# Performance work log

Measured on AMD Instinct MI355X. Metric: run time of the kernel, lower is better.

The kernel has to match this reference:

```python
import jax, jax.numpy as jnp
import numpy as np

N, B, H, L0, L1, C = 196608, 4096, 230, 10, 53, 53


def setup_inputs() -> dict:
    key = jax.random.key(0)
    ks = jax.random.split(key, 12)
    x = jax.random.normal(ks[0], (N, H), jnp.float32)
    label_index = jax.random.randint(ks[1], (N,), 0, C, dtype=jnp.int32)
    rl0 = jax.random.randint(ks[2], (C, 1), 0, L0, dtype=jnp.int32)
    rl1 = jax.random.randint(ks[3], (C, 1), 0, L1, dtype=jnp.int32)
    relation_levels = jnp.concatenate([rl0, rl1], axis=1)  # [C, 2]
    # equal-size bags: 4096 bags of 48 sentences (ragged boundaries)
    scope = (jnp.arange(B + 1, dtype=jnp.int32) * (N // B))
    rel_emb0 = jax.random.normal(ks[4], (L0, H), jnp.float32)
    rel_emb1 = jax.random.normal(ks[5], (L1, H), jnp.float32)
    att_w0 = jax.random.normal(ks[6], (L0,), jnp.float32)
    att_w1 = jax.random.normal(ks[7], (L1,), jnp.float32)
    w_s = jax.random.normal(ks[8], (2, 3 * H), jnp.float32) * 0.05
    b_s = jax.random.normal(ks[9], (2, 1), jnp.float32) * 0.05
    disc_matrix = jax.random.normal(ks[10], (C, 2 * H), jnp.float32) * 0.05
    bias = jnp.zeros((C,), jnp.float32)
    return {"x": x, "rel_emb0": rel_emb0, "rel_emb1": rel_emb1,
            "att_w0": att_w0, "att_w1": att_w1, "w_s": w_s, "b_s": b_s,
            "disc_matrix": disc_matrix, "bias": bias,
            "label_index": label_index, "relation_levels": relation_levels,
            "scope": scope}


def _segment_softmax(logits, seg, num_seg):
    # logits: [N]; stable softmax within each bag (segment)
    m = jax.ops.segment_max(logits, seg, num_segments=num_seg)
    e = jnp.exp(logits - m[seg])
    z = jax.ops.segment_sum(e, seg, num_segments=num_seg)
    return e / z[seg]


def reference(x, rel_emb0, rel_emb1, att_w0, att_w1, w_s, b_s, disc_matrix,
              bias, label_index, relation_levels, scope):
    n, h = x.shape
    num_bags = scope.shape[0] - 1
    # bag id of each sentence from ragged boundaries
    seg = jnp.searchsorted(scope, jnp.arange(n, dtype=scope.dtype), side="right") - 1

    ll = relation_levels[label_index]                 # [N, 2]
    r0 = rel_emb0[ll[:, 0]]                           # [N, H]
    r1 = rel_emb1[ll[:, 1]]                           # [N, H]
    s = jnp.tanh(jnp.concatenate([x, r0, r1], axis=-1))  # [N, 3H]
    logits = w_s @ s.T + b_s                          # [2, N]

    # per-bag ragged softmax over sentences, per hierarchy level
    score = jax.vmap(lambda l: _segment_softmax(l, seg, num_bags))(logits)  # [2, N]

    # vertical (hierarchy) attention: softmax over hier per sentence, mean per bag
    v = jnp.stack([att_w0[ll[:, 0]], att_w1[ll[:, 1]]])  # [2, N]
    vsm = jax.nn.softmax(v, axis=0)                      # [2, N]
    counts = jax.ops.segment_sum(jnp.ones((n,), x.dtype), seg, num_segments=num_bags)
    layer_att = jax.vmap(lambda r: jax.ops.segment_sum(r, seg, num_segments=num_bags))(vsm) / counts  # [2, B]

    # attention-weighted bag representation: per bag, [2, len] @ [len, H]
    rep = jax.vmap(lambda sc: jax.ops.segment_sum(sc[:, None] * x, seg, num_segments=num_bags))(score)  # [2, B, H]
    tower = (layer_att[:, :, None] * rep).transpose(1, 0, 2).reshape(num_bags, 2 * h)  # [B, 2H]

    return tower @ disc_matrix.T + bias  # [B, C]
```

## Files before the change

### kernel.cpp

```cpp
#include <hip/hip_runtime.h>

#define NTOT 196608
#define BAGS 4096
#define H 230
#define H3 690
#define NC 53

__device__ __forceinline__ float fast_tanh(float x) {
    float e = __expf(2.f * x);
    float r = __builtin_amdgcn_rcpf(e + 1.f);
    return fmaf(-2.f, r, 1.f);
}

__global__ void class_table_kernel(const float* __restrict__ rel_emb0,
                                   const float* __restrict__ rel_emb1,
                                   const float* __restrict__ att_w0,
                                   const float* __restrict__ att_w1,
                                   const float* __restrict__ w_s,
                                   const float* __restrict__ b_s,
                                   const int* __restrict__ relation_levels,
                                   float* __restrict__ cls)
{
    int c = blockIdx.x;
    int lane = threadIdx.x;
    int l0 = relation_levels[c * 2 + 0];
    int l1 = relation_levels[c * 2 + 1];
    float a00 = 0.f, a01 = 0.f, a10 = 0.f, a11 = 0.f;
    for (int j = lane; j < H; j += 64) {
        float t0 = fast_tanh(rel_emb0[l0 * H + j]);
        float t1 = fast_tanh(rel_emb1[l1 * H + j]);
        a00 += w_s[0 * H3 + H + j] * t0;
        a01 += w_s[0 * H3 + 2 * H + j] * t1;
        a10 += w_s[1 * H3 + H + j] * t0;
        a11 += w_s[1 * H3 + 2 * H + j] * t1;
    }
    for (int m = 32; m; m >>= 1) {
        a00 += __shfl_xor(a00, m);
        a01 += __shfl_xor(a01, m);
        a10 += __shfl_xor(a10, m);
        a11 += __shfl_xor(a11, m);
    }
    if (lane == 0) {
        cls[0 * NC + c] = a00 + a01 + b_s[0];
        cls[1 * NC + c] = a10 + a11 + b_s[1];
        float v0 = att_w0[l0], v1 = att_w1[l1];
        float mx = fmaxf(v0, v1);
        float e0 = __expf(v0 - mx), e1 = __expf(v1 - mx);
        float rz = __builtin_amdgcn_rcpf(e0 + e1);
        cls[2 * NC + c] = e0 * rz;
        cls[3 * NC + c] = e1 * rz;
    }
}

__global__ __launch_bounds__(256, 8) void bag_kernel(
    const float* __restrict__ x,
    const float* __restrict__ w_s,
    const float* __restrict__ disc,
    const float* __restrict__ bias,
    const int* __restrict__ label_index,
    const int* __restrict__ scope,
    const float* __restrict__ cls,
    float* __restrict__ out)
{
    __shared__ __align__(16) float part[4][464];
    __shared__ float zs[4][4];
    __shared__ __align__(16) float t01[464];

    int b = blockIdx.x;
    int start = scope[b];
    int cnt = scope[b + 1] - start;
    int tid = threadIdx.x;
    int wave = tid >> 6;
    int lane = tid & 63;
    const float* xb = x + (long long)start * H;

    float w0r[4], w1r[4];
#pragma unroll
    for (int u = 0; u < 4; ++u) {
        int jj = lane + 64 * u;
        w0r[u] = (jj < H) ? w_s[jj] : 0.f;
        w1r[u] = (jj < H) ? w_s[H3 + jj] : 0.f;
    }

    float acc0[4] = {0.f, 0.f, 0.f, 0.f};
    float acc1[4] = {0.f, 0.f, 0.f, 0.f};
    float z0 = 0.f, z1 = 0.f, sv0 = 0.f, sv1 = 0.f;

    for (int t = 0; t < 12; ++t) {
        int i = wave + 4 * t;
        if (i >= cnt) break;
        const float* row = xb + i * H;
        float r[4];
        float d0 = 0.f, d1 = 0.f;
#pragma unroll
        for (int u = 0; u < 4; ++u) {
            int jj = lane + 64 * u;
            r[u] = (jj < H) ? row[jj] : 0.f;
        }
#pragma unroll
        for (int u = 0; u < 4; ++u) {
            float tnh = fast_tanh(r[u]);
            d0 += w0r[u] * tnh;
            d1 += w1r[u] * tnh;
        }
#pragma unroll
        for (int m = 32; m; m >>= 1) {
            d0 += __shfl_xor(d0, m);
            d1 += __shfl_xor(d1, m);
        }
        int c = label_index[start + i];
        float e0 = __expf(d0 + cls[c]);
        float e1 = __expf(d1 + cls[NC + c]);
        z0 += e0; z1 += e1;
        sv0 += cls[2 * NC + c];
        sv1 += cls[3 * NC + c];
#pragma unroll
        for (int u = 0; u < 4; ++u) {
            acc0[u] = fmaf(e0, r[u], acc0[u]);
            acc1[u] = fmaf(e1, r[u], acc1[u]);
        }
    }

#pragma unroll
    for (int u = 0; u < 4; ++u) {
        int jj = lane + 64 * u;
        if (jj < H) {
            part[wave][jj]     = acc0[u];
            part[wave][H + jj] = acc1[u];
        }
    }
    if (lane == 0) {
        zs[wave][0] = z0; zs[wave][1] = z1;
        zs[wave][2] = sv0; zs[wave][3] = sv1;
    }
    __syncthreads();

    float zt0 = zs[0][0] + zs[1][0] + zs[2][0] + zs[3][0];
    float zt1 = zs[0][1] + zs[1][1] + zs[2][1] + zs[3][1];
    float st0 = zs[0][2] + zs[1][2] + zs[2][2] + zs[3][2];
    float st1 = zs[0][3] + zs[1][3] + zs[2][3] + zs[3][3];
    float rc  = __builtin_amdgcn_rcpf((float)cnt);
    float s0  = st0 * rc * __builtin_amdgcn_rcpf(zt0);
    float s1  = st1 * rc * __builtin_amdgcn_rcpf(zt1);

    for (int t = tid; t < 2 * H; t += 256) {
        float s = part[0][t] + part[1][t] + part[2][t] + part[3][t];
        t01[t] = s * (t < H ? s0 : s1);
    }
    __syncthreads();

    int q = tid & 3;
    int c = tid >> 2;
    if (c < NC) {
        const float4* drow4 = (const float4*)(disc + c * (2 * H));
        const float4* t4 = (const float4*)t01;
        float acc = 0.f;
        for (int k = q; k < 115; k += 4) {
            float4 dv = drow4[k];
            float4 tv = t4[k];
            acc += dv.x * tv.x + dv.y * tv.y + dv.z * tv.z + dv.w * tv.w;
        }
        acc += __shfl_down(acc, 2, 4);
        acc += __shfl_down(acc, 1, 4);
        if (q == 0) out[b * NC + c] = acc + bias[c];
    }
}

extern "C" void kernel_launch(void* const* d_in, const int* in_sizes, int n_in,
                              void* d_out, int out_size, void* d_ws, size_t ws_size,
                              hipStream_t stream) {
    const float* x               = (const float*)d_in[0];
    const float* rel_emb0        = (const float*)d_in[1];
    const float* rel_emb1        = (const float*)d_in[2];
    const float* att_w0          = (const float*)d_in[3];
    const float* att_w1          = (const float*)d_in[4];
    const float* w_s             = (const float*)d_in[5];
    const float* b_s             = (const float*)d_in[6];
    const float* disc            = (const float*)d_in[7];
    const float* bias            = (const float*)d_in[8];
    const int*   label_index     = (const int*)d_in[9];
    const int*   relation_levels = (const int*)d_in[10];
    const int*   scope           = (const int*)d_in[11];
    float* out = (float*)d_out;
    float* cls = (float*)d_ws;

    class_table_kernel<<<NC, 64, 0, stream>>>(rel_emb0, rel_emb1, att_w0, att_w1,
                                              w_s, b_s, relation_levels, cls);
    bag_kernel<<<BAGS, 256, 0, stream>>>(x, w_s, disc, bias, label_index, scope,
                                         cls, out);
}
```

Measured before the change: 301.3 us.

## Vectorize row loads as float2 and software-pipeline rows for full bags

Rows of x are now loaded as float2 (two contiguous elements per lane) instead of four strided scalar loads. For bags of exactly 48 sentences, the loop is fully unrolled and prefetches rows two iterations ahead, overlapping memory latency with the tanh/dot/reduction work. Other bag sizes use a simple loop. Occupancy hint drops from 8 to 6 blocks per SM to make room for the extra prefetch registers. Float2 loads rely on the row stride (230 floats) keeping 8-byte alignment, which holds since 230 is even.

```diff
diff --git a/kernel.cpp b/kernel.cpp
--- a/kernel.cpp
+++ b/kernel.cpp
@@ -52,7 +52,7 @@
     }
 }
 
-__global__ __launch_bounds__(256, 8) void bag_kernel(
+__global__ __launch_bounds__(256, 6) void bag_kernel(
     const float* __restrict__ x,
     const float* __restrict__ w_s,
     const float* __restrict__ disc,
@@ -74,60 +74,78 @@
     int lane = tid & 63;
     const float* xb = x + (long long)start * H;
 
-    float w0r[4], w1r[4];
-#pragma unroll
-    for (int u = 0; u < 4; ++u) {
-        int jj = lane + 64 * u;
-        w0r[u] = (jj < H) ? w_s[jj] : 0.f;
-        w1r[u] = (jj < H) ? w_s[H3 + jj] : 0.f;
-    }
-
-    float acc0[4] = {0.f, 0.f, 0.f, 0.f};
-    float acc1[4] = {0.f, 0.f, 0.f, 0.f};
+    const float2* w0p = (const float2*)w_s;
+    const float2* w1p = (const float2*)(w_s + H3);
+    float2 w0a = w0p[lane];
+    float2 w1a = w1p[lane];
+    float2 w0b = make_float2(0.f, 0.f), w1b = make_float2(0.f, 0.f);
+    if (lane < 51) { w0b = w0p[64 + lane]; w1b = w1p[64 + lane]; }
+
+    float2 acc0[2] = { make_float2(0.f, 0.f), make_float2(0.f, 0.f) };
+    float2 acc1[2] = { make_float2(0.f, 0.f), make_float2(0.f, 0.f) };
     float z0 = 0.f, z1 = 0.f, sv0 = 0.f, sv1 = 0.f;
 
-    for (int t = 0; t < 12; ++t) {
-        int i = wave + 4 * t;
-        if (i >= cnt) break;
-        const float* row = xb + i * H;
-        float r[4];
-        float d0 = 0.f, d1 = 0.f;
-#pragma unroll
-        for (int u = 0; u < 4; ++u) {
-            int jj = lane + 64 * u;
-            r[u] = (jj < H) ? row[jj] : 0.f;
-        }
-#pragma unroll
-        for (int u = 0; u < 4; ++u) {
-            float tnh = fast_tanh(r[u]);
-            d0 += w0r[u] * tnh;
-            d1 += w1r[u] * tnh;
-        }
+    auto load_row = [&](int i, float2& a, float2& bb, int& c) {
+        const float2* row2 = (const float2*)(xb + i * H);
+        a = row2[lane];
+        bb = (lane < 51) ? row2[64 + lane] : make_float2(0.f, 0.f);
+        c = label_index[start + i];
+    };
+
+    auto body = [&](float2 a, float2 bb, int c) {
+        float t0 = fast_tanh(a.x);
+        float t1 = fast_tanh(a.y);
+        float t2 = fast_tanh(bb.x);
+        float t3 = fast_tanh(bb.y);
+        float d0 = w0a.x * t0 + w0a.y * t1 + w0b.x * t2 + w0b.y * t3;
+        float d1 = w1a.x * t0 + w1a.y * t1 + w1b.x * t2 + w1b.y * t3;
 #pragma unroll
         for (int m = 32; m; m >>= 1) {
             d0 += __shfl_xor(d0, m);
             d1 += __shfl_xor(d1, m);
         }
-        int c = label_index[start + i];
         float e0 = __expf(d0 + cls[c]);
         float e1 = __expf(d1 + cls[NC + c]);
         z0 += e0; z1 += e1;
         sv0 += cls[2 * NC + c];
         sv1 += cls[3 * NC + c];
+        acc0[0].x = fmaf(e0, a.x,  acc0[0].x);
+        acc0[0].y = fmaf(e0, a.y,  acc0[0].y);
+        acc0[1].x = fmaf(e0, bb.x, acc0[1].x);
+        acc0[1].y = fmaf(e0, bb.y, acc0[1].y);
+        acc1[0].x = fmaf(e1, a.x,  acc1[0].x);
+        acc1[0].y = fmaf(e1, a.y,  acc1[0].y);
+        acc1[1].x = fmaf(e1, bb.x, acc1[1].x);
+        acc1[1].y = fmaf(e1, bb.y, acc1[1].y);
+    };
+
+    if (cnt == 48) {
+        float2 a0, b0, a1, b1;
+        float2 a2 = make_float2(0.f, 0.f), b2 = make_float2(0.f, 0.f);
+        int c0, c1, c2 = 0;
+        load_row(wave,     a0, b0, c0);
+        load_row(wave + 4, a1, b1, c1);
 #pragma unroll
-        for (int u = 0; u < 4; ++u) {
-            acc0[u] = fmaf(e0, r[u], acc0[u]);
-            acc1[u] = fmaf(e1, r[u], acc1[u]);
-        }
-    }
-
-#pragma unroll
-    for (int u = 0; u < 4; ++u) {
-        int jj = lane + 64 * u;
-        if (jj < H) {
-            part[wave][jj]     = acc0[u];
-            part[wave][H + jj] = acc1[u];
-        }
+        for (int t = 0; t < 12; ++t) {
+            if (t + 2 < 12) load_row(wave + 4 * (t + 2), a2, b2, c2);
+            body(a0, b0, c0);
+            a0 = a1; b0 = b1; c0 = c1;
+            a1 = a2; b1 = b2; c1 = c2;
+        }
+    } else {
+        for (int i = wave; i < cnt; i += 4) {
+            float2 a, bb; int c;
+            load_row(i, a, bb, c);
+            body(a, bb, c);
+        }
+    }
+
+    float2* pw = (float2*)part[wave];
+    pw[lane]       = acc0[0];
+    pw[115 + lane] = acc1[0];
+    if (lane < 51) {
+        pw[64 + lane]        = acc0[1];
+        pw[115 + 64 + lane]  = acc1[1];
     }
     if (lane == 0) {
         zs[wave][0] = z0; zs[wave][1] = z1;
```

Result: slower. 400.4 us (+32.9%).

## Batch all row loads up front with float2 vectorization and grouped shuffle reductions

Applied to the files above, without the earlier changes.

Rows are now read as float2 (115 pairs per row, two per lane). When a bag holds 48 rows, a fast path issues all 12 row loads per wave and the label loads before any compute, then processes rows in groups of 4 so the butterfly shuffle reductions of several rows are interleaved. The aim is more loads in flight per wave to hide HBM latency, fewer load instructions, and overlapped shuffle latency. The cost is many more registers, so launch bounds drop from 8 to 4 blocks per SM to permit lower occupancy.

```diff
diff --git a/kernel.cpp b/kernel.cpp
--- a/kernel.cpp
+++ b/kernel.cpp
@@ -52,7 +52,7 @@
     }
 }
 
-__global__ __launch_bounds__(256, 8) void bag_kernel(
+__global__ __launch_bounds__(256, 4) void bag_kernel(
     const float* __restrict__ x,
     const float* __restrict__ w_s,
     const float* __restrict__ disc,
@@ -74,60 +74,102 @@
     int lane = tid & 63;
     const float* xb = x + (long long)start * H;
 
-    float w0r[4], w1r[4];
-#pragma unroll
-    for (int u = 0; u < 4; ++u) {
-        int jj = lane + 64 * u;
-        w0r[u] = (jj < H) ? w_s[jj] : 0.f;
-        w1r[u] = (jj < H) ? w_s[H3 + jj] : 0.f;
-    }
-
-    float acc0[4] = {0.f, 0.f, 0.f, 0.f};
-    float acc1[4] = {0.f, 0.f, 0.f, 0.f};
+    const float2* w0p = (const float2*)w_s;
+    const float2* w1p = (const float2*)(w_s + H3);
+    float2 w0a = w0p[lane];
+    float2 w1a = w1p[lane];
+    float2 w0b = make_float2(0.f, 0.f), w1b = make_float2(0.f, 0.f);
+    if (lane < 51) { w0b = w0p[64 + lane]; w1b = w1p[64 + lane]; }
+
+    float2 acc0a = make_float2(0.f, 0.f), acc0b = make_float2(0.f, 0.f);
+    float2 acc1a = make_float2(0.f, 0.f), acc1b = make_float2(0.f, 0.f);
     float z0 = 0.f, z1 = 0.f, sv0 = 0.f, sv1 = 0.f;
 
-    for (int t = 0; t < 12; ++t) {
-        int i = wave + 4 * t;
-        if (i >= cnt) break;
-        const float* row = xb + i * H;
-        float r[4];
-        float d0 = 0.f, d1 = 0.f;
-#pragma unroll
-        for (int u = 0; u < 4; ++u) {
-            int jj = lane + 64 * u;
-            r[u] = (jj < H) ? row[jj] : 0.f;
-        }
-#pragma unroll
-        for (int u = 0; u < 4; ++u) {
-            float tnh = fast_tanh(r[u]);
-            d0 += w0r[u] * tnh;
-            d1 += w1r[u] * tnh;
-        }
-#pragma unroll
-        for (int m = 32; m; m >>= 1) {
-            d0 += __shfl_xor(d0, m);
-            d1 += __shfl_xor(d1, m);
-        }
-        int c = label_index[start + i];
-        float e0 = __expf(d0 + cls[c]);
-        float e1 = __expf(d1 + cls[NC + c]);
-        z0 += e0; z1 += e1;
-        sv0 += cls[2 * NC + c];
-        sv1 += cls[3 * NC + c];
-#pragma unroll
-        for (int u = 0; u < 4; ++u) {
-            acc0[u] = fmaf(e0, r[u], acc0[u]);
-            acc1[u] = fmaf(e1, r[u], acc1[u]);
-        }
-    }
-
-#pragma unroll
-    for (int u = 0; u < 4; ++u) {
-        int jj = lane + 64 * u;
-        if (jj < H) {
-            part[wave][jj]     = acc0[u];
-            part[wave][H + jj] = acc1[u];
-        }
+    if (cnt == 48) {
+        int cl[12];
+#pragma unroll
+        for (int t = 0; t < 12; ++t)
+            cl[t] = label_index[start + wave + 4 * t];
+
+        float2 ra[12], rb[12];
+#pragma unroll
+        for (int t = 0; t < 12; ++t) {
+            const float2* r2 = (const float2*)(xb + (wave + 4 * t) * H);
+            ra[t] = r2[lane];
+            rb[t] = (lane < 51) ? r2[64 + lane] : make_float2(0.f, 0.f);
+        }
+
+#pragma unroll
+        for (int g = 0; g < 3; ++g) {
+            float d0[4], d1[4];
+#pragma unroll
+            for (int k = 0; k < 4; ++k) {
+                int t = 4 * g + k;
+                float t0 = fast_tanh(ra[t].x), t1 = fast_tanh(ra[t].y);
+                float t2 = fast_tanh(rb[t].x), t3 = fast_tanh(rb[t].y);
+                d0[k] = w0a.x * t0 + w0a.y * t1 + w0b.x * t2 + w0b.y * t3;
+                d1[k] = w1a.x * t0 + w1a.y * t1 + w1b.x * t2 + w1b.y * t3;
+            }
+#pragma unroll
+            for (int m = 32; m; m >>= 1) {
+#pragma unroll
+                for (int k = 0; k < 4; ++k) {
+                    d0[k] += __shfl_xor(d0[k], m);
+                    d1[k] += __shfl_xor(d1[k], m);
+                }
+            }
+#pragma unroll
+            for (int k = 0; k < 4; ++k) {
+                int t = 4 * g + k;
+                int c = cl[t];
+                float e0 = __expf(d0[k] + cls[c]);
+                float e1 = __expf(d1[k] + cls[NC + c]);
+                z0 += e0; z1 += e1;
+                sv0 += cls[2 * NC + c];
+                sv1 += cls[3 * NC + c];
+                acc0a.x = fmaf(e0, ra[t].x, acc0a.x);
+                acc0a.y = fmaf(e0, ra[t].y, acc0a.y);
+                acc0b.x = fmaf(e0, rb[t].x, acc0b.x);
+                acc0b.y = fmaf(e0, rb[t].y, acc0b.y);
+                acc1a.x = fmaf(e1, ra[t].x, acc1a.x);
+                acc1a.y = fmaf(e1, ra[t].y, acc1a.y);
+                acc1b.x = fmaf(e1, rb[t].x, acc1b.x);
+                acc1b.y = fmaf(e1, rb[t].y, acc1b.y);
+            }
+        }
+    } else {
+        for (int i = wave; i < cnt; i += 4) {
+            const float2* r2 = (const float2*)(xb + (long long)i * H);
+            float2 a = r2[lane];
+            float2 bb = (lane < 51) ? r2[64 + lane] : make_float2(0.f, 0.f);
+            float t0 = fast_tanh(a.x), t1 = fast_tanh(a.y);
+            float t2 = fast_tanh(bb.x), t3 = fast_tanh(bb.y);
+            float d0 = w0a.x * t0 + w0a.y * t1 + w0b.x * t2 + w0b.y * t3;
+            float d1 = w1a.x * t0 + w1a.y * t1 + w1b.x * t2 + w1b.y * t3;
+#pragma unroll
+            for (int m = 32; m; m >>= 1) {
+                d0 += __shfl_xor(d0, m);
+                d1 += __shfl_xor(d1, m);
+            }
+            int c = label_index[start + i];
+            float e0 = __expf(d0 + cls[c]);
+            float e1 = __expf(d1 + cls[NC + c]);
+            z0 += e0; z1 += e1;
+            sv0 += cls[2 * NC + c];
+            sv1 += cls[3 * NC + c];
+            acc0a.x = fmaf(e0, a.x,  acc0a.x); acc0a.y = fmaf(e0, a.y,  acc0a.y);
+            acc0b.x = fmaf(e0, bb.x, acc0b.x); acc0b.y = fmaf(e0, bb.y, acc0b.y);
+            acc1a.x = fmaf(e1, a.x,  acc1a.x); acc1a.y = fmaf(e1, a.y,  acc1a.y);
+            acc1b.x = fmaf(e1, bb.x, acc1b.x); acc1b.y = fmaf(e1, bb.y, acc1b.y);
+        }
+    }
+
+    float2* pw = (float2*)part[wave];
+    pw[lane]       = acc0a;
+    pw[115 + lane] = acc1a;
+    if (lane < 51) {
+        pw[64 + lane]       = acc0b;
+        pw[115 + 64 + lane] = acc1b;
     }
     if (lane == 0) {
         zs[wave][0] = z0; zs[wave][1] = z1;
```

New measurement: 303.3 us. Within noise of the previous version (+0.7%).

## Process two bag rows per wave with half-wave lanes and swizzle reductions

Applied to the files above, without the earlier changes.

Each wave now splits into two 32-lane halves that work on different sentences at once. Each lane loads 8 contiguous floats of a row as float2 values and owns 8 accumulators. The per-row dot product is reduced inside each half-wave with ds_swizzle butterflies, and the per-class table is packed into one float4 per class so a single load fetches it. The aim is more independent row loads in flight and fewer shuffle steps per row. In exchange it uses more registers, wastes some lanes on padding beyond column 230, and masks tail rows when a bag has an odd number of rows per wave.

```diff
diff --git a/kernel.cpp b/kernel.cpp
--- a/kernel.cpp
+++ b/kernel.cpp
@@ -5,6 +5,9 @@
 #define H 230
 #define H3 690
 #define NC 53
+
+#define SWZ_ADD(v, pat) \
+    ((v) + __int_as_float(__builtin_amdgcn_ds_swizzle(__float_as_int(v), (pat))))
 
 __device__ __forceinline__ float fast_tanh(float x) {
     float e = __expf(2.f * x);
@@ -41,14 +44,16 @@
         a11 += __shfl_xor(a11, m);
     }
     if (lane == 0) {
-        cls[0 * NC + c] = a00 + a01 + b_s[0];
-        cls[1 * NC + c] = a10 + a11 + b_s[1];
         float v0 = att_w0[l0], v1 = att_w1[l1];
         float mx = fmaxf(v0, v1);
         float e0 = __expf(v0 - mx), e1 = __expf(v1 - mx);
         float rz = __builtin_amdgcn_rcpf(e0 + e1);
-        cls[2 * NC + c] = e0 * rz;
-        cls[3 * NC + c] = e1 * rz;
+        float4 v;
+        v.x = a00 + a01 + b_s[0];
+        v.y = a10 + a11 + b_s[1];
+        v.z = e0 * rz;
+        v.w = e1 * rz;
+        ((float4*)cls)[c] = v;
     }
 }
 
@@ -62,76 +67,95 @@
     const float* __restrict__ cls,
     float* __restrict__ out)
 {
-    __shared__ __align__(16) float part[4][464];
+    __shared__ __align__(16) float part[4][2][2][256];
     __shared__ float zs[4][4];
     __shared__ __align__(16) float t01[464];
 
     int b = blockIdx.x;
-    int start = scope[b];
-    int cnt = scope[b + 1] - start;
     int tid = threadIdx.x;
     int wave = tid >> 6;
     int lane = tid & 63;
-    const float* xb = x + (long long)start * H;
-
-    float w0r[4], w1r[4];
-#pragma unroll
-    for (int u = 0; u < 4; ++u) {
-        int jj = lane + 64 * u;
-        w0r[u] = (jj < H) ? w_s[jj] : 0.f;
-        w1r[u] = (jj < H) ? w_s[H3 + jj] : 0.f;
-    }
-
-    float acc0[4] = {0.f, 0.f, 0.f, 0.f};
-    float acc1[4] = {0.f, 0.f, 0.f, 0.f};
+    int half = lane >> 5;
+    int hl   = lane & 31;
+
+    int start = __builtin_amdgcn_readfirstlane(scope[b]);
+    int cnt   = __builtin_amdgcn_readfirstlane(scope[b + 1]) - start;
+
+    int j0 = 8 * hl;
+    int i0 = (j0 >> 1);
+    int i1 = i0 + 1, i2 = i0 + 2, i3 = i0 + 3;
+    if (i0 > 114) i0 = 114;
+    if (i1 > 114) i1 = 114;
+    if (i2 > 114) i2 = 114;
+    if (i3 > 114) i3 = 114;
+
+    float w0r[8], w1r[8];
+#pragma unroll
+    for (int k = 0; k < 8; ++k) {
+        int j = j0 + k;
+        w0r[k] = (j < H) ? w_s[j] : 0.f;
+        w1r[k] = (j < H) ? w_s[H3 + j] : 0.f;
+    }
+
+    float acc0[8], acc1[8];
+#pragma unroll
+    for (int k = 0; k < 8; ++k) { acc0[k] = 0.f; acc1[k] = 0.f; }
     float z0 = 0.f, z1 = 0.f, sv0 = 0.f, sv1 = 0.f;
 
-    for (int t = 0; t < 12; ++t) {
-        int i = wave + 4 * t;
-        if (i >= cnt) break;
-        const float* row = xb + i * H;
-        float r[4];
+    const float4* cls4 = (const float4*)cls;
+
+    for (int m = 0; wave + 8 * m < cnt; ++m) {
+        int rMine = wave + 8 * m + 4 * half;
+        int valid = (rMine < cnt);
+        int rq = valid ? rMine : (cnt - 1);
+
+        const float2* rp = (const float2*)(x + (long long)(start + rq) * H);
+        float2 v0 = rp[i0], v1 = rp[i1], v2 = rp[i2], v3 = rp[i3];
+        int c = label_index[start + rq];
+        float4 cv = cls4[c];
+
+        float r[8] = { v0.x, v0.y, v1.x, v1.y, v2.x, v2.y, v3.x, v3.y };
         float d0 = 0.f, d1 = 0.f;
 #pragma unroll
-        for (int u = 0; u < 4; ++u) {
-            int jj = lane + 64 * u;
-            r[u] = (jj < H) ? row[jj] : 0.f;
+        for (int k = 0; k < 8; ++k) {
+            float th = fast_tanh(r[k]);
+            d0 += w0r[k] * th;
+            d1 += w1r[k] * th;
         }
-#pragma unroll
-        for (int u = 0; u < 4; ++u) {
-            float tnh = fast_tanh(r[u]);
-            d0 += w0r[u] * tnh;
-            d1 += w1r[u] * tnh;
+        d0 = SWZ_ADD(d0, 0x041F); d1 = SWZ_ADD(d1, 0x041F);
+        d0 = SWZ_ADD(d0, 0x081F); d1 = SWZ_ADD(d1, 0x081F);
+        d0 = SWZ_ADD(d0, 0x101F); d1 = SWZ_ADD(d1, 0x101F);
+        d0 = SWZ_ADD(d0, 0x201F); d1 = SWZ_ADD(d1, 0x201F);
+        d0 = SWZ_ADD(d0, 0x401F); d1 = SWZ_ADD(d1, 0x401F);
+
+        float e0 = __expf(d0 + cv.x);
+        float e1 = __expf(d1 + cv.y);
+        e0 = valid ? e0 : 0.f;
+        e1 = valid ? e1 : 0.f;
+        z0 += e0; z1 += e1;
+        sv0 += valid ? cv.z : 0.f;
+        sv1 += valid ? cv.w : 0.f;
+#pragma unroll
+        for (int k = 0; k < 8; ++k) {
+            acc0[k] = fmaf(e0, r[k], acc0[k]);
+            acc1[k] = fmaf(e1, r[k], acc1[k]);
         }
-#pragma unroll
-        for (int m = 32; m; m >>= 1) {
-            d0 += __shfl_xor(d0, m);
-            d1 += __shfl_xor(d1, m);
-        }
-        int c = label_index[start + i];
-        float e0 = __expf(d0 + cls[c]);
-        float e1 = __expf(d1 + cls[NC + c]);
-        z0 += e0; z1 += e1;
-        sv0 += cls[2 * NC + c];
-        sv1 += cls[3 * NC + c];
-#pragma unroll
-        for (int u = 0; u < 4; ++u) {
-            acc0[u] = fmaf(e0, r[u], acc0[u]);
-            acc1[u] = fmaf(e1, r[u], acc1[u]);
-        }
-    }
-
-#pragma unroll
-    for (int u = 0; u < 4; ++u) {
-        int jj = lane + 64 * u;
-        if (jj < H) {
-            part[wave][jj]     = acc0[u];
-            part[wave][H + jj] = acc1[u];
-        }
-    }
+    }
+
+    z0  += __shfl_xor(z0, 32);  z1  += __shfl_xor(z1, 32);
+    sv0 += __shfl_xor(sv0, 32); sv1 += __shfl_xor(sv1, 32);
     if (lane == 0) {
         zs[wave][0] = z0; zs[wave][1] = z1;
         zs[wave][2] = sv0; zs[wave][3] = sv1;
+    }
+
+    {
+        float4* p0 = (float4*)&part[wave][half][0][8 * hl];
+        float4* p1 = (float4*)&part[wave][half][1][8 * hl];
+        p0[0] = make_float4(acc0[0], acc0[1], acc0[2], acc0[3]);
+        p0[1] = make_float4(acc0[4], acc0[5], acc0[6], acc0[7]);
+        p1[0] = make_float4(acc1[0], acc1[1], acc1[2], acc1[3]);
+        p1[1] = make_float4(acc1[4], acc1[5], acc1[6], acc1[7]);
     }
     __syncthreads();
 
@@ -144,8 +168,13 @@
     float s1  = st1 * rc * __builtin_amdgcn_rcpf(zt1);
 
     for (int t = tid; t < 2 * H; t += 256) {
-        float s = part[0][t] + part[1][t] + part[2][t] + part[3][t];
-        t01[t] = s * (t < H ? s0 : s1);
+        int ch = (t >= H);
+        int c  = t - ch * H;
+        float s = part[0][0][ch][c] + part[0][1][ch][c]
+                + part[1][0][ch][c] + part[1][1][ch][c]
+                + part[2][0][ch][c] + part[2][1][ch][c]
+                + part[3][0][ch][c] + part[3][1][ch][c];
+        t01[t] = s * (ch ? s1 : s0);
     }
     __syncthreads();
 
```

After: 329.4 us. 9.3% more time.
